# Kernel optimization log

Hardware: AMD Instinct MI355X
Metric: run time of the kernel (lower is better)

Reference implementation:

```python
import jax, jax.numpy as jnp
import numpy as np

EPS = 1e-5

def _ln(x, g, b):
    mu = jnp.mean(x, axis=-1, keepdims=True)
    var = jnp.mean((x - mu) ** 2, axis=-1, keepdims=True)
    return (x - mu) * jax.lax.rsqrt(var + EPS) * g + b

def setup_inputs() -> dict:
    key = jax.random.key(0)
    B, V, I, H = 32, 48, 24, 768
    ks = jax.random.split(key, 10)
    s = 0.02
    return {
        'variables': jax.random.normal(ks[0], (B, V, H), jnp.float32),
        'interventions': jax.random.normal(ks[1], (B, I, H), jnp.float32),
        # variable_encoder: Linear(H,H) + LayerNorm(H)
        'W_enc': jax.random.normal(ks[2], (H, H), jnp.float32) * s,
        'b_enc': jnp.zeros((H,), jnp.float32),
        'g_enc': jnp.ones((H,), jnp.float32),
        'be_enc': jnp.zeros((H,), jnp.float32),
        # graph_generator: Linear(2H,H) + LN(H) + ReLU + Linear(H,1) + Sigmoid
        'Wg1': jax.random.normal(ks[3], (2 * H, H), jnp.float32) * s,
        'bg1': jnp.zeros((H,), jnp.float32),
        'g_g': jnp.ones((H,), jnp.float32),
        'b_g': jnp.zeros((H,), jnp.float32),
        'Wg2': jax.random.normal(ks[4], (H, 1), jnp.float32) * s,
        'bg2': jnp.zeros((1,), jnp.float32),
        # intervention_predictor: Linear(2H,H) + LN(H) + ReLU + Linear(H,H)
        'Wi1': jax.random.normal(ks[5], (2 * H, H), jnp.float32) * s,
        'bi1': jnp.zeros((H,), jnp.float32),
        'g_i': jnp.ones((H,), jnp.float32),
        'b_i': jnp.zeros((H,), jnp.float32),
        'Wi2': jax.random.normal(ks[6], (H, H), jnp.float32) * s,
        'bi2': jnp.zeros((H,), jnp.float32),
    }

def reference(variables, interventions, W_enc, b_enc, g_enc, be_enc,
              Wg1, bg1, g_g, b_g, Wg2, bg2, Wi1, bi1, g_i, b_i, Wi2, bi2):
    H = variables.shape[-1]
    V = variables.shape[1]
    # variable encoder: Linear + LayerNorm + ReLU
    enc = jax.nn.relu(_ln(variables @ W_enc + b_enc, g_enc, be_enc))  # [B,V,H]

    # graph generator over all ordered pairs (i,j): concat([enc_i, enc_j]) @ Wg1
    # split Wg1 so the concat-matmul becomes two small GEMMs + broadcast add
    hi = jnp.einsum('bvh,hk->bvk', enc, Wg1[:H])   # contribution of enc_i
    hj = jnp.einsum('bvh,hk->bvk', enc, Wg1[H:])   # contribution of enc_j
    h = jax.nn.relu(_ln(hi[:, :, None, :] + hj[:, None, :, :] + bg1, g_g, b_g))  # [B,V,V,H]
    score = jax.nn.sigmoid(jnp.squeeze(h @ Wg2, -1) + bg2[0])  # [B,V,V]
    # diagonal (i==j) is never written in the original -> stays zero
    causal_graph = score * (1.0 - jnp.eye(V, dtype=score.dtype))

    # intervention predictor: concat([intervention_i, enc_j]) -> MLP
    ha = jnp.einsum('bih,hk->bik', interventions, Wi1[:H])  # [B,I,H]
    hb = jnp.einsum('bvh,hk->bvk', enc, Wi1[H:])            # [B,V,H]
    h2 = jax.nn.relu(_ln(ha[:, :, None, :] + hb[:, None, :, :] + bi1, g_i, b_i))  # [B,I,V,H]
    effects = h2 @ Wi2 + bi2  # [B,I,V,H]

    return (effects, causal_graph, enc)
```

## Files before the change

### kernel.cpp

```cpp
#include <hip/hip_runtime.h>
#include <math.h>

#define Bp 32
#define Vp 48
#define Ip 24
#define Hp 768
#define EPS 1e-5f

#define EFFECTS_SIZE (Bp*Ip*Vp*Hp)
#define GRAPH_SIZE   (Bp*Vp*Vp)
#define ENC_SIZE     (Bp*Vp*Hp)
#define MS           (Hp*Hp)

typedef __attribute__((ext_vector_type(8))) short short8;
typedef __attribute__((ext_vector_type(4))) float floatx4;
typedef __attribute__((ext_vector_type(2))) float floatx2;
typedef __attribute__((ext_vector_type(4))) unsigned int uintx4;

__device__ __forceinline__ unsigned short f2bf(float f) {
    unsigned int u = __float_as_uint(f);
    u += 0x7fffu + ((u >> 16) & 1u);
    return (unsigned short)(u >> 16);
}
__device__ __forceinline__ unsigned int f2bf2(float a, float b) {
    return (unsigned int)f2bf(a) | ((unsigned int)f2bf(b) << 16);
}

__device__ __forceinline__ uintx4 ln8(floatx4 xa, floatx4 xb, float mu, float rs,
                                      floatx4 ga, floatx4 gb, floatx4 ba, floatx4 bb)
{
    float y0 = fmaxf((xa.x - mu) * rs * ga.x + ba.x, 0.f);
    float y1 = fmaxf((xa.y - mu) * rs * ga.y + ba.y, 0.f);
    float y2 = fmaxf((xa.z - mu) * rs * ga.z + ba.z, 0.f);
    float y3 = fmaxf((xa.w - mu) * rs * ga.w + ba.w, 0.f);
    float y4 = fmaxf((xb.x - mu) * rs * gb.x + bb.x, 0.f);
    float y5 = fmaxf((xb.y - mu) * rs * gb.y + bb.y, 0.f);
    float y6 = fmaxf((xb.z - mu) * rs * gb.z + bb.z, 0.f);
    float y7 = fmaxf((xb.w - mu) * rs * gb.w + bb.w, 0.f);
    uintx4 v;
    v.x = f2bf2(y0, y1); v.y = f2bf2(y2, y3);
    v.z = f2bf2(y4, y5); v.w = f2bf2(y6, y7);
    return v;
}

__global__ __launch_bounds__(256) void pack_weights(
    const float* __restrict__ W_enc, const float* __restrict__ Wg1,
    const float* __restrict__ Wi1, const float* __restrict__ Wi2,
    unsigned short* __restrict__ packed)
{
    const int bid = blockIdx.x;
    const int m = bid / 288;
    const int rem = bid - m * 288;
    const int T = rem / 6;
    const int u = rem - T * 6;
    const float* src;
    switch (m) {
        case 0: src = W_enc; break;
        case 1: src = Wg1; break;
        case 2: src = Wg1 + Hp * Hp; break;
        case 3: src = Wi1 + Hp * Hp; break;
        case 4: src = Wi1; break;
        default: src = Wi2; break;
    }
    unsigned short* dst = packed + (size_t)m * MS;
    const int lane = threadIdx.x & 63;
    const int kq = threadIdx.x >> 6;
    const int col = T * 16 + (lane & 15);
    const int krow0 = (lane >> 4) * 8;
    const int kb = kq + 4 * u;
    unsigned int w[4];
#pragma unroll
    for (int p2 = 0; p2 < 4; ++p2) {
        float f0 = src[(size_t)(kb * 32 + krow0 + 2 * p2)     * Hp + col];
        float f1 = src[(size_t)(kb * 32 + krow0 + 2 * p2 + 1) * Hp + col];
        w[p2] = f2bf2(f0, f1);
    }
    uintx4 v; v.x = w[0]; v.y = w[1]; v.z = w[2]; v.w = w[3];
    *(uintx4*)(dst + ((size_t)(T * 24 + kb) * 64 + lane) * 8) = v;
}

__global__ __launch_bounds__(256) void convert_inputs(
    const float* __restrict__ vars, const float* __restrict__ intv,
    const float* __restrict__ bg1, const float* __restrict__ bi1,
    unsigned short* __restrict__ varb, unsigned short* __restrict__ intvb,
    float* __restrict__ bias2304)
{
    const int p = blockIdx.x * 256 + threadIdx.x;
    const int VPn = ENC_SIZE / 2;
    if (p < VPn) {
        float2 f = ((const float2*)vars)[p];
        ((unsigned int*)varb)[p] = f2bf2(f.x, f.y);
    } else {
        int q = p - VPn;
        float2 f = ((const float2*)intv)[q];
        ((unsigned int*)intvb)[q] = f2bf2(f.x, f.y);
    }
    if (blockIdx.x == 0) {
        for (int t = threadIdx.x; t < 2304; t += 256)
            bias2304[t] = (t < 768) ? 0.0f : (t < 1536 ? bg1[t - 768] : bi1[t - 1536]);
    }
}

__global__ __launch_bounds__(256) void gemm32(
    const unsigned short* __restrict__ A, const unsigned short* __restrict__ Bpk,
    const float* __restrict__ bias, float* __restrict__ C, int ldc)
{
    __shared__ unsigned short Asl[2 * 24 * 64 * 8];
    const int tid = threadIdx.x, wave = tid >> 6, lane = tid & 63;
    const int m0 = blockIdx.x * 32;

#pragma unroll
    for (int uu = 0; uu < 12; ++uu) {
        const int s = tid + 256 * uu;
        const int mt = s / 1536;
        const int r2 = s - mt * 1536;
        const int kb = r2 >> 6;
        const int L  = r2 & 63;
        uintx4 v = *(const uintx4*)(A + (size_t)(m0 + mt * 16 + (L & 15)) * Hp
                                      + kb * 32 + (L >> 4) * 8);
        *(uintx4*)(&Asl[((mt * 24 + kb) * 64 + (L ^ (kb & 7))) * 8]) = v;
    }
    __syncthreads();

    const int mrow = lane & 15, kq = lane >> 4;
    const int rot = ((blockIdx.x * 5 + blockIdx.y) & 7) * 3;
    const int wavep = (wave + blockIdx.x) & 3;
    const int Tg0 = blockIdx.y * 12 + wavep * 3;
    const unsigned short* Bbase = Bpk + (size_t)Tg0 * 12288 + lane * 8;

    const floatx4 z = {0.f, 0.f, 0.f, 0.f};
    floatx4 acc[2][3];
#pragma unroll
    for (int mt = 0; mt < 2; ++mt)
#pragma unroll
        for (int nt = 0; nt < 3; ++nt) acc[mt][nt] = z;

    short8 bbuf[4][3], abuf[2][2];
#pragma unroll
    for (int d = 0; d < 3; ++d) {
        int kc = d + rot; if (kc >= 24) kc -= 24;
#pragma unroll
        for (int nt = 0; nt < 3; ++nt)
            bbuf[d][nt] = *(const short8*)(Bbase + (size_t)nt * 12288 + kc * 512);
    }
    {
        int kc = rot;
#pragma unroll
        for (int mt = 0; mt < 2; ++mt)
            abuf[0][mt] = *(const short8*)(&Asl[((mt * 24 + kc) * 64 + (lane ^ (kc & 7))) * 8]);
    }

#pragma unroll
    for (int kb = 0; kb < 24; ++kb) {
        if (kb + 3 < 24) {
            int kc = kb + 3 + rot; if (kc >= 24) kc -= 24;
#pragma unroll
            for (int nt = 0; nt < 3; ++nt)
                bbuf[(kb + 3) & 3][nt] =
                    *(const short8*)(Bbase + (size_t)nt * 12288 + kc * 512);
        }
        if (kb + 1 < 24) {
            int kc = kb + 1 + rot; if (kc >= 24) kc -= 24;
#pragma unroll
            for (int mt = 0; mt < 2; ++mt)
                abuf[(kb + 1) & 1][mt] = *(const short8*)(
                    &Asl[((mt * 24 + kc) * 64 + (lane ^ (kc & 7))) * 8]);
        }
        __builtin_amdgcn_s_setprio(1);
#pragma unroll
        for (int mt = 0; mt < 2; ++mt)
#pragma unroll
            for (int nt = 0; nt < 3; ++nt)
                acc[mt][nt] = __builtin_amdgcn_mfma_f32_16x16x32_bf16(
                    abuf[kb & 1][mt], bbuf[kb & 3][nt], acc[mt][nt], 0, 0, 0);
        __builtin_amdgcn_s_setprio(0);
    }

#pragma unroll
    for (int nt = 0; nt < 3; ++nt) {
        const int colg = (Tg0 + nt) * 16 + mrow;
        const float bv = bias ? bias[colg] : 0.0f;
#pragma unroll
        for (int mt = 0; mt < 2; ++mt)
#pragma unroll
            for (int r = 0; r < 4; ++r)
                C[(size_t)(m0 + mt * 16 + kq * 4 + r) * ldc + colg] = acc[mt][nt][r] + bv;
    }
}

__global__ __launch_bounds__(256) void ln_relu(
    const float* __restrict__ pre, const float* __restrict__ g,
    const float* __restrict__ be, float* __restrict__ encf,
    unsigned short* __restrict__ encb)
{
    const int wave = threadIdx.x >> 6, lane = threadIdx.x & 63;
    const int row = blockIdx.x * 4 + wave;
    const float2* rp = (const float2*)(pre + (size_t)row * Hp);
    float2 x[6]; float s = 0.f, q = 0.f;
#pragma unroll
    for (int c = 0; c < 6; ++c) {
        x[c] = rp[lane + 64 * c];
        s += x[c].x + x[c].y;
        q += x[c].x * x[c].x + x[c].y * x[c].y;
    }
#pragma unroll
    for (int m = 1; m < 64; m <<= 1) { s += __shfl_xor(s, m, 64); q += __shfl_xor(q, m, 64); }
    const float mu = s * (1.0f / Hp);
    const float var = q * (1.0f / Hp) - mu * mu;
    const float rs = rsqrtf(var + EPS);
    floatx2* of = (floatx2*)(encf + (size_t)row * Hp);
    unsigned int* ob = (unsigned int*)(encb + (size_t)row * Hp);
#pragma unroll
    for (int c = 0; c < 6; ++c) {
        const float2 g2 = ((const float2*)g)[lane + 64 * c];
        const float2 b2 = ((const float2*)be)[lane + 64 * c];
        float y0 = fmaxf((x[c].x - mu) * rs * g2.x + b2.x, 0.f);
        float y1 = fmaxf((x[c].y - mu) * rs * g2.y + b2.y, 0.f);
        floatx2 y; y.x = y0; y.y = y1;
        __builtin_nontemporal_store(y, &of[lane + 64 * c]);
        ob[lane + 64 * c] = f2bf2(y0, y1);
    }
}

__global__ __launch_bounds__(256) void graph_kernel(
    const float* __restrict__ ws2, const float* __restrict__ gg_,
    const float* __restrict__ bb_, const float* __restrict__ Wg2,
    const float* __restrict__ bg2, float* __restrict__ out)
{
    const int wave = threadIdx.x >> 6, lane = threadIdx.x & 63;
    const int p = blockIdx.x;
    const int b = p / Vp, i = p - b * Vp;
    const floatx4* hi4 = (const floatx4*)(ws2 + (size_t)p * 2304);
    const floatx4* gg4 = (const floatx4*)gg_;
    const floatx4* bb4 = (const floatx4*)bb_;
    const floatx4* w24 = (const floatx4*)Wg2;
    floatx4 ri[3], gg[3], bb[3], w2[3];
#pragma unroll
    for (int c = 0; c < 3; ++c) {
        const int k = lane + 64 * c;
        ri[c] = hi4[k]; gg[c] = gg4[k]; bb[c] = bb4[k]; w2[c] = w24[k];
    }
    const float bg2v = bg2[0];
    const int j0 = wave * 12;
    for (int jj = 0; jj < 12; jj += 2) {
        const int jA = j0 + jj, jB = jA + 1;
        const floatx4* hjA = (const floatx4*)(ws2 + (size_t)(b * Vp + jA) * 2304 + 768);
        const floatx4* hjB = (const floatx4*)(ws2 + (size_t)(b * Vp + jB) * 2304 + 768);
        floatx4 xA[3], xB[3];
        float sA = 0.f, qA = 0.f, sB = 0.f, qB = 0.f;
#pragma unroll
        for (int c = 0; c < 3; ++c) {
            const int k = lane + 64 * c;
            xA[c] = ri[c] + hjA[k];
            xB[c] = ri[c] + hjB[k];
            sA += xA[c].x + xA[c].y + xA[c].z + xA[c].w;
            qA += xA[c].x * xA[c].x + xA[c].y * xA[c].y + xA[c].z * xA[c].z + xA[c].w * xA[c].w;
            sB += xB[c].x + xB[c].y + xB[c].z + xB[c].w;
            qB += xB[c].x * xB[c].x + xB[c].y * xB[c].y + xB[c].z * xB[c].z + xB[c].w * xB[c].w;
        }
#pragma unroll
        for (int m = 1; m < 64; m <<= 1) {
            sA += __shfl_xor(sA, m, 64); qA += __shfl_xor(qA, m, 64);
            sB += __shfl_xor(sB, m, 64); qB += __shfl_xor(qB, m, 64);
        }
        const float muA = sA * (1.0f / Hp);
        const float rsA = rsqrtf(qA * (1.0f / Hp) - muA * muA + EPS);
        const float muB = sB * (1.0f / Hp);
        const float rsB = rsqrtf(qB * (1.0f / Hp) - muB * muB + EPS);
        float pdA = 0.f, pdB = 0.f;
#pragma unroll
        for (int c = 0; c < 3; ++c) {
            float yA0 = fmaxf((xA[c].x - muA) * rsA * gg[c].x + bb[c].x, 0.f);
            float yA1 = fmaxf((xA[c].y - muA) * rsA * gg[c].y + bb[c].y, 0.f);
            float yA2 = fmaxf((xA[c].z - muA) * rsA * gg[c].z + bb[c].z, 0.f);
            float yA3 = fmaxf((xA[c].w - muA) * rsA * gg[c].w + bb[c].w, 0.f);
            pdA = fmaf(yA0, w2[c].x, pdA); pdA = fmaf(yA1, w2[c].y, pdA);
            pdA = fmaf(yA2, w2[c].z, pdA); pdA = fmaf(yA3, w2[c].w, pdA);
            float yB0 = fmaxf((xB[c].x - muB) * rsB * gg[c].x + bb[c].x, 0.f);
            float yB1 = fmaxf((xB[c].y - muB) * rsB * gg[c].y + bb[c].y, 0.f);
            float yB2 = fmaxf((xB[c].z - muB) * rsB * gg[c].z + bb[c].z, 0.f);
            float yB3 = fmaxf((xB[c].w - muB) * rsB * gg[c].w + bb[c].w, 0.f);
            pdB = fmaf(yB0, w2[c].x, pdB); pdB = fmaf(yB1, w2[c].y, pdB);
            pdB = fmaf(yB2, w2[c].z, pdB); pdB = fmaf(yB3, w2[c].w, pdB);
        }
#pragma unroll
        for (int m = 1; m < 64; m <<= 1) {
            pdA += __shfl_xor(pdA, m, 64);
            pdB += __shfl_xor(pdB, m, 64);
        }
        if (lane == 0) {
            float scA = (i == jA) ? 0.0f : 1.0f / (1.0f + expf(-(pdA + bg2v)));
            float scB = (i == jB) ? 0.0f : 1.0f / (1.0f + expf(-(pdB + bg2v)));
            out[(size_t)p * Vp + jA] = scA;
            out[(size_t)p * Vp + jB] = scB;
        }
    }
}

__global__ __launch_bounds__(512, 2) void effects96(
    const float* __restrict__ ha, const float* __restrict__ ws2,
    const float* __restrict__ g_i, const float* __restrict__ b_i,
    const unsigned short* __restrict__ Bpk, const float* __restrict__ bi2,
    float* __restrict__ out)
{
    __shared__ unsigned short Asl[6 * 24 * 64 * 8];
    const int tid = threadIdx.x, wave = tid >> 6, lane = tid & 63;
    const int bid = blockIdx.x;
    const int pair = bid >> 1, nhalf = bid & 1;
    const int b = pair / 12;
    const int bi0 = b * Ip + (pair - b * 12) * 2;
    const int half = lane >> 5, hl = lane & 31;

    {
        const floatx4* ha0 = (const floatx4*)(ha + (size_t)bi0 * Hp);
        const floatx4* ha1 = (const floatx4*)(ha + (size_t)(bi0 + 1) * Hp);
        const floatx4* gp = (const floatx4*)g_i;
        const floatx4* bp = (const floatx4*)b_i;
        floatx4 hv0[6], hv1[6], gv[6], bv[6];
#pragma unroll
        for (int t = 0; t < 3; ++t) {
            hv0[2*t] = ha0[2*hl + 64*t];  hv0[2*t+1] = ha0[2*hl + 1 + 64*t];
            hv1[2*t] = ha1[2*hl + 64*t];  hv1[2*t+1] = ha1[2*hl + 1 + 64*t];
            gv[2*t]  = gp[2*hl + 64*t];   gv[2*t+1]  = gp[2*hl + 1 + 64*t];
            bv[2*t]  = bp[2*hl + 64*t];   bv[2*t+1]  = bp[2*hl + 1 + 64*t];
        }

#pragma unroll
        for (int p = 0; p < 3; ++p) {
            const int j = wave * 6 + 2 * p + half;
            const floatx4* hbp = (const floatx4*)(ws2 + (size_t)(b * Vp + j) * 2304 + 1536);
            floatx4 x0[6], x1[6];
            float s0 = 0.f, q0 = 0.f, s1 = 0.f, q1 = 0.f;
#pragma unroll
            for (int t = 0; t < 3; ++t) {
                const floatx4 hA = hbp[2*hl + 64*t];
                const floatx4 hB = hbp[2*hl + 1 + 64*t];
                x0[2*t]   = hv0[2*t]   + hA;  x0[2*t+1] = hv0[2*t+1] + hB;
                x1[2*t]   = hv1[2*t]   + hA;  x1[2*t+1] = hv1[2*t+1] + hB;
            }
#pragma unroll
            for (int c = 0; c < 6; ++c) {
                s0 += x0[c].x + x0[c].y + x0[c].z + x0[c].w;
                q0 += x0[c].x*x0[c].x + x0[c].y*x0[c].y + x0[c].z*x0[c].z + x0[c].w*x0[c].w;
                s1 += x1[c].x + x1[c].y + x1[c].z + x1[c].w;
                q1 += x1[c].x*x1[c].x + x1[c].y*x1[c].y + x1[c].z*x1[c].z + x1[c].w*x1[c].w;
            }
#pragma unroll
            for (int m = 1; m < 32; m <<= 1) {
                s0 += __shfl_xor(s0, m, 64); q0 += __shfl_xor(q0, m, 64);
                s1 += __shfl_xor(s1, m, 64); q1 += __shfl_xor(q1, m, 64);
            }
            const float mu0 = s0 * (1.0f / Hp);
            const float rs0 = rsqrtf(q0 * (1.0f / Hp) - mu0 * mu0 + EPS);
            const float mu1 = s1 * (1.0f / Hp);
            const float rs1 = rsqrtf(q1 * (1.0f / Hp) - mu1 * mu1 + EPS);
            const int mt0 = j >> 4, mt1 = 3 + mt0, mr = j & 15;
#pragma unroll
            for (int t = 0; t < 3; ++t) {
                const int cpk = hl + 32 * t;
                const int kb = cpk >> 2, kq2 = cpk & 3;
                const int swz = (kq2 * 16 + mr) ^ (kb & 7);
                uintx4 v0 = ln8(x0[2*t], x0[2*t+1], mu0, rs0,
                                gv[2*t], gv[2*t+1], bv[2*t], bv[2*t+1]);
                *(uintx4*)(&Asl[((mt0 * 24 + kb) * 64 + swz) * 8]) = v0;
                uintx4 v1 = ln8(x1[2*t], x1[2*t+1], mu1, rs1,
                                gv[2*t], gv[2*t+1], bv[2*t], bv[2*t+1]);
                *(uintx4*)(&Asl[((mt1 * 24 + kb) * 64 + swz) * 8]) = v1;
            }
        }
    }
    __syncthreads();

    const int mrow = lane & 15, kq = lane >> 4;
    const int rot = (pair & 7) * 3;
    const int wavep = (wave + pair) & 7;
    const int Tg0 = nhalf * 24 + wavep * 3;
    const unsigned short* Bbase = Bpk + (size_t)Tg0 * 12288 + lane * 8;

    const floatx4 z = {0.f, 0.f, 0.f, 0.f};
    floatx4 acc[6][3];
#pragma unroll
    for (int mt = 0; mt < 6; ++mt)
#pragma unroll
        for (int nt = 0; nt < 3; ++nt) acc[mt][nt] = z;

    short8 bbuf[4][3], abuf[2][6];
#pragma unroll
    for (int d = 0; d < 3; ++d) {
        int kc = d + rot; if (kc >= 24) kc -= 24;
#pragma unroll
        for (int nt = 0; nt < 3; ++nt)
            bbuf[d][nt] = *(const short8*)(Bbase + (size_t)nt * 12288 + kc * 512);
    }
    {
        int kc = rot;
#pragma unroll
        for (int mt = 0; mt < 6; ++mt)
            abuf[0][mt] = *(const short8*)(&Asl[((mt * 24 + kc) * 64 + (lane ^ (kc & 7))) * 8]);
    }

#pragma unroll
    for (int kb = 0; kb < 24; ++kb) {
        if (kb + 3 < 24) {
            int kc = kb + 3 + rot; if (kc >= 24) kc -= 24;
#pragma unroll
            for (int nt = 0; nt < 3; ++nt)
                bbuf[(kb + 3) & 3][nt] =
                    *(const short8*)(Bbase + (size_t)nt * 12288 + kc * 512);
        }
        if (kb + 1 < 24) {
            int kc = kb + 1 + rot; if (kc >= 24) kc -= 24;
#pragma unroll
            for (int mt = 0; mt < 6; ++mt)
                abuf[(kb + 1) & 1][mt] = *(const short8*)(
                    &Asl[((mt * 24 + kc) * 64 + (lane ^ (kc & 7))) * 8]);
        }
        __builtin_amdgcn_s_setprio(1);
#pragma unroll
        for (int mt = 0; mt < 6; ++mt)
#pragma unroll
            for (int nt = 0; nt < 3; ++nt)
                acc[mt][nt] = __builtin_amdgcn_mfma_f32_16x16x32_bf16(
                    abuf[kb & 1][mt], bbuf[kb & 3][nt], acc[mt][nt], 0, 0, 0);
        __builtin_amdgcn_s_setprio(0);
    }

#pragma unroll
    for (int nt = 0; nt < 3; ++nt) {
        const int colg = (Tg0 + nt) * 16 + mrow;
        const float biasv = bi2[colg];
#pragma unroll
        for (int mt = 0; mt < 6; ++mt) {
#pragma unroll
            for (int r = 0; r < 4; ++r) {
                const int rr = mt * 16 + kq * 4 + r;
                __builtin_nontemporal_store(
                    acc[mt][nt][r] + biasv,
                    &out[(size_t)(bi0 * 48 + rr) * Hp + colg]);
            }
        }
    }
}

extern "C" void kernel_launch(void* const* d_in, const int* in_sizes, int n_in,
                              void* d_out, int out_size, void* d_ws, size_t ws_size,
                              hipStream_t stream) {
    const float* variables     = (const float*)d_in[0];
    const float* interventions = (const float*)d_in[1];
    const float* W_enc  = (const float*)d_in[2];
    const float* b_enc  = (const float*)d_in[3];
    const float* g_enc  = (const float*)d_in[4];
    const float* be_enc = (const float*)d_in[5];
    const float* Wg1 = (const float*)d_in[6];
    const float* bg1 = (const float*)d_in[7];
    const float* g_g = (const float*)d_in[8];
    const float* b_g = (const float*)d_in[9];
    const float* Wg2 = (const float*)d_in[10];
    const float* bg2 = (const float*)d_in[11];
    const float* Wi1 = (const float*)d_in[12];
    const float* bi1 = (const float*)d_in[13];
    const float* g_i = (const float*)d_in[14];
    const float* b_i = (const float*)d_in[15];
    const float* Wi2 = (const float*)d_in[16];
    const float* bi2 = (const float*)d_in[17];

    float* out = (float*)d_out;
    float* effects = out;
    float* graph = out + EFFECTS_SIZE;
    float* enc_f = out + EFFECTS_SIZE + GRAPH_SIZE;

    char* wsb = (char*)d_ws;
    unsigned short* packedW = (unsigned short*)wsb;
    float* ws2  = (float*)(wsb + 7077888);
    float* pre1 = ws2;
    float* ha   = (float*)(wsb + 7077888 + 14155776);
    unsigned short* varb  = (unsigned short*)(wsb + 23592960);
    unsigned short* intvb = (unsigned short*)(wsb + 25952256);
    unsigned short* encb  = (unsigned short*)(wsb + 27131904);
    float* bias2304 = (float*)(wsb + 29491200);

    pack_weights<<<1728, 256, 0, stream>>>(W_enc, Wg1, Wi1, Wi2, packedW);
    convert_inputs<<<3456, 256, 0, stream>>>(variables, interventions, bg1, bi1,
                                             varb, intvb, bias2304);
    gemm32<<<dim3(48, 4), 256, 0, stream>>>(varb, packedW, b_enc, pre1, Hp);
    ln_relu<<<384, 256, 0, stream>>>(pre1, g_enc, be_enc, enc_f, encb);
    gemm32<<<dim3(48, 12), 256, 0, stream>>>(encb, packedW + (size_t)1 * MS,
                                             bias2304, ws2, 2304);
    gemm32<<<dim3(24, 4), 256, 0, stream>>>(intvb, packedW + (size_t)4 * MS,
                                            nullptr, ha, Hp);
    graph_kernel<<<Bp * Vp, 256, 0, stream>>>(ws2, g_g, b_g, Wg2, bg2, graph);
    effects96<<<768, 512, 0, stream>>>(ha, ws2, g_i, b_i,
                                       packedW + (size_t)5 * MS, bi2, effects);
}
```

Before: 279.4 us.

## Merge encoder and intervention GEMMs into one launch; rewrite graph kernel with LDS tiling

The intervention GEMM, which does not depend on the encoder output, now runs in the same launch as the encoder GEMM through a combined grid, saving a kernel launch and letting the two fill the GPU together. The graph scorer is rebuilt so each block handles 6 i-rows of one batch and stages the hj rows in swizzled shared memory. Each lane then computes one (i,j) pair instead of one wave per pair with shuffle reductions. This trades the shuffle overhead for repeated LDS passes and fewer, larger blocks (256 blocks, 48 of 64 lanes active).

```diff
diff --git a/kernel.cpp b/kernel.cpp
--- a/kernel.cpp
+++ b/kernel.cpp
@@ -101,13 +101,14 @@
     }
 }
 
-__global__ __launch_bounds__(256) void gemm32(
+__device__ __forceinline__ void gemm32_body(
+    unsigned short* Asl,
     const unsigned short* __restrict__ A, const unsigned short* __restrict__ Bpk,
-    const float* __restrict__ bias, float* __restrict__ C, int ldc)
-{
-    __shared__ unsigned short Asl[2 * 24 * 64 * 8];
+    const float* __restrict__ bias, float* __restrict__ C, int ldc,
+    int bx, int by)
+{
     const int tid = threadIdx.x, wave = tid >> 6, lane = tid & 63;
-    const int m0 = blockIdx.x * 32;
+    const int m0 = bx * 32;
 
 #pragma unroll
     for (int uu = 0; uu < 12; ++uu) {
@@ -123,9 +124,9 @@
     __syncthreads();
 
     const int mrow = lane & 15, kq = lane >> 4;
-    const int rot = ((blockIdx.x * 5 + blockIdx.y) & 7) * 3;
-    const int wavep = (wave + blockIdx.x) & 3;
-    const int Tg0 = blockIdx.y * 12 + wavep * 3;
+    const int rot = ((bx * 5 + by) & 7) * 3;
+    const int wavep = (wave + bx) & 3;
+    const int Tg0 = by * 12 + wavep * 3;
     const unsigned short* Bbase = Bpk + (size_t)Tg0 * 12288 + lane * 8;
 
     const floatx4 z = {0.f, 0.f, 0.f, 0.f};
@@ -185,6 +186,29 @@
 #pragma unroll
             for (int r = 0; r < 4; ++r)
                 C[(size_t)(m0 + mt * 16 + kq * 4 + r) * ldc + colg] = acc[mt][nt][r] + bv;
+    }
+}
+
+__global__ __launch_bounds__(256) void gemm32(
+    const unsigned short* __restrict__ A, const unsigned short* __restrict__ Bpk,
+    const float* __restrict__ bias, float* __restrict__ C, int ldc)
+{
+    __shared__ unsigned short Asl[2 * 24 * 64 * 8];
+    gemm32_body(Asl, A, Bpk, bias, C, ldc, blockIdx.x, blockIdx.y);
+}
+
+__global__ __launch_bounds__(256) void gemm32_pair(
+    const unsigned short* __restrict__ A1, const unsigned short* __restrict__ B1,
+    const float* __restrict__ bias1, float* __restrict__ C1,
+    const unsigned short* __restrict__ A2, const unsigned short* __restrict__ B2,
+    float* __restrict__ C2)
+{
+    __shared__ unsigned short Asl[2 * 24 * 64 * 8];
+    if (blockIdx.y < 4) {
+        gemm32_body(Asl, A1, B1, bias1, C1, Hp, blockIdx.x, blockIdx.y);
+    } else {
+        if (blockIdx.x >= 24) return;
+        gemm32_body(Asl, A2, B2, nullptr, C2, Hp, blockIdx.x, blockIdx.y - 4);
     }
 }
 
@@ -222,78 +246,92 @@
     }
 }
 
-__global__ __launch_bounds__(256) void graph_kernel(
+__global__ __launch_bounds__(384) void graph_v2(
     const float* __restrict__ ws2, const float* __restrict__ gg_,
     const float* __restrict__ bb_, const float* __restrict__ Wg2,
     const float* __restrict__ bg2, float* __restrict__ out)
 {
-    const int wave = threadIdx.x >> 6, lane = threadIdx.x & 63;
-    const int p = blockIdx.x;
-    const int b = p / Vp, i = p - b * Vp;
-    const floatx4* hi4 = (const floatx4*)(ws2 + (size_t)p * 2304);
-    const floatx4* gg4 = (const floatx4*)gg_;
-    const floatx4* bb4 = (const floatx4*)bb_;
-    const floatx4* w24 = (const floatx4*)Wg2;
-    floatx4 ri[3], gg[3], bb[3], w2[3];
-#pragma unroll
-    for (int c = 0; c < 3; ++c) {
-        const int k = lane + 64 * c;
-        ri[c] = hi4[k]; gg[c] = gg4[k]; bb[c] = bb4[k]; w2[c] = w24[k];
-    }
-    const float bg2v = bg2[0];
-    const int j0 = wave * 12;
-    for (int jj = 0; jj < 12; jj += 2) {
-        const int jA = j0 + jj, jB = jA + 1;
-        const floatx4* hjA = (const floatx4*)(ws2 + (size_t)(b * Vp + jA) * 2304 + 768);
-        const floatx4* hjB = (const floatx4*)(ws2 + (size_t)(b * Vp + jB) * 2304 + 768);
-        floatx4 xA[3], xB[3];
-        float sA = 0.f, qA = 0.f, sB = 0.f, qB = 0.f;
-#pragma unroll
-        for (int c = 0; c < 3; ++c) {
-            const int k = lane + 64 * c;
-            xA[c] = ri[c] + hjA[k];
-            xB[c] = ri[c] + hjB[k];
-            sA += xA[c].x + xA[c].y + xA[c].z + xA[c].w;
-            qA += xA[c].x * xA[c].x + xA[c].y * xA[c].y + xA[c].z * xA[c].z + xA[c].w * xA[c].w;
-            sB += xB[c].x + xB[c].y + xB[c].z + xB[c].w;
-            qB += xB[c].x * xB[c].x + xB[c].y * xB[c].y + xB[c].z * xB[c].z + xB[c].w * xB[c].w;
-        }
-#pragma unroll
-        for (int m = 1; m < 64; m <<= 1) {
-            sA += __shfl_xor(sA, m, 64); qA += __shfl_xor(qA, m, 64);
-            sB += __shfl_xor(sB, m, 64); qB += __shfl_xor(qB, m, 64);
-        }
-        const float muA = sA * (1.0f / Hp);
-        const float rsA = rsqrtf(qA * (1.0f / Hp) - muA * muA + EPS);
-        const float muB = sB * (1.0f / Hp);
-        const float rsB = rsqrtf(qB * (1.0f / Hp) - muB * muB + EPS);
-        float pdA = 0.f, pdB = 0.f;
-#pragma unroll
-        for (int c = 0; c < 3; ++c) {
-            float yA0 = fmaxf((xA[c].x - muA) * rsA * gg[c].x + bb[c].x, 0.f);
-            float yA1 = fmaxf((xA[c].y - muA) * rsA * gg[c].y + bb[c].y, 0.f);
-            float yA2 = fmaxf((xA[c].z - muA) * rsA * gg[c].z + bb[c].z, 0.f);
-            float yA3 = fmaxf((xA[c].w - muA) * rsA * gg[c].w + bb[c].w, 0.f);
-            pdA = fmaf(yA0, w2[c].x, pdA); pdA = fmaf(yA1, w2[c].y, pdA);
-            pdA = fmaf(yA2, w2[c].z, pdA); pdA = fmaf(yA3, w2[c].w, pdA);
-            float yB0 = fmaxf((xB[c].x - muB) * rsB * gg[c].x + bb[c].x, 0.f);
-            float yB1 = fmaxf((xB[c].y - muB) * rsB * gg[c].y + bb[c].y, 0.f);
-            float yB2 = fmaxf((xB[c].z - muB) * rsB * gg[c].z + bb[c].z, 0.f);
-            float yB3 = fmaxf((xB[c].w - muB) * rsB * gg[c].w + bb[c].w, 0.f);
-            pdB = fmaf(yB0, w2[c].x, pdB); pdB = fmaf(yB1, w2[c].y, pdB);
-            pdB = fmaf(yB2, w2[c].z, pdB); pdB = fmaf(yB3, w2[c].w, pdB);
-        }
-#pragma unroll
-        for (int m = 1; m < 64; m <<= 1) {
-            pdA += __shfl_xor(pdA, m, 64);
-            pdB += __shfl_xor(pdB, m, 64);
-        }
-        if (lane == 0) {
-            float scA = (i == jA) ? 0.0f : 1.0f / (1.0f + expf(-(pdA + bg2v)));
-            float scB = (i == jB) ? 0.0f : 1.0f / (1.0f + expf(-(pdB + bg2v)));
-            out[(size_t)p * Vp + jA] = scA;
-            out[(size_t)p * Vp + jB] = scB;
-        }
+    __shared__ floatx4 HJ[96 * 64];
+    __shared__ floatx4 HI[6 * 192];
+    __shared__ floatx4 Gc[192];
+    __shared__ floatx4 Bc[192];
+    __shared__ floatx4 W2c[192];
+    const int tid = threadIdx.x, wave = tid >> 6, lane = tid & 63;
+    const int b = blockIdx.x >> 3, ig = blockIdx.x & 7;
+    const floatx4* w4 = (const floatx4*)ws2;
+
+    for (int idx = tid; idx < 6 * 192; idx += 384) {
+        const int i = idx / 192, c = idx - i * 192;
+        HI[idx] = w4[(size_t)(b * 48 + ig * 6 + i) * 576 + c];
+    }
+    for (int c = tid; c < 192; c += 384) {
+        Gc[c]  = ((const floatx4*)gg_)[c];
+        Bc[c]  = ((const floatx4*)bb_)[c];
+        W2c[c] = ((const floatx4*)Wg2)[c];
+    }
+    for (int idx = tid; idx < 48 * 96; idx += 384) {
+        const int j = idx / 96, c = idx - j * 96;
+        HJ[c * 64 + (j ^ (c & 7))] = w4[(size_t)(b * 48 + j) * 576 + 192 + c];
+    }
+    __syncthreads();
+
+    float s = 0.f, q = 0.f, pd = 0.f, mu = 0.f, rs = 0.f;
+
+    if (lane < 48) {
+#pragma unroll 4
+        for (int c = 0; c < 96; ++c) {
+            const floatx4 x = HI[wave * 192 + c] + HJ[c * 64 + (lane ^ (c & 7))];
+            s += x.x + x.y + x.z + x.w;
+            q += x.x * x.x + x.y * x.y + x.z * x.z + x.w * x.w;
+        }
+    }
+    __syncthreads();
+    for (int idx = tid; idx < 48 * 96; idx += 384) {
+        const int j = idx / 96, c = idx - j * 96;
+        HJ[c * 64 + (j ^ (c & 7))] = w4[(size_t)(b * 48 + j) * 576 + 192 + 96 + c];
+    }
+    __syncthreads();
+
+    if (lane < 48) {
+#pragma unroll 4
+        for (int c = 0; c < 96; ++c) {
+            const floatx4 x = HI[wave * 192 + 96 + c] + HJ[c * 64 + (lane ^ (c & 7))];
+            s += x.x + x.y + x.z + x.w;
+            q += x.x * x.x + x.y * x.y + x.z * x.z + x.w * x.w;
+        }
+        mu = s * (1.0f / Hp);
+        rs = rsqrtf(q * (1.0f / Hp) - mu * mu + EPS);
+#pragma unroll 2
+        for (int c = 0; c < 96; ++c) {
+            const floatx4 x = HI[wave * 192 + 96 + c] + HJ[c * 64 + (lane ^ (c & 7))];
+            const floatx4 g = Gc[96 + c], b2 = Bc[96 + c], w = W2c[96 + c];
+            pd += fmaxf((x.x - mu) * rs * g.x + b2.x, 0.f) * w.x;
+            pd += fmaxf((x.y - mu) * rs * g.y + b2.y, 0.f) * w.y;
+            pd += fmaxf((x.z - mu) * rs * g.z + b2.z, 0.f) * w.z;
+            pd += fmaxf((x.w - mu) * rs * g.w + b2.w, 0.f) * w.w;
+        }
+    }
+    __syncthreads();
+    for (int idx = tid; idx < 48 * 96; idx += 384) {
+        const int j = idx / 96, c = idx - j * 96;
+        HJ[c * 64 + (j ^ (c & 7))] = w4[(size_t)(b * 48 + j) * 576 + 192 + c];
+    }
+    __syncthreads();
+
+    if (lane < 48) {
+#pragma unroll 2
+        for (int c = 0; c < 96; ++c) {
+            const floatx4 x = HI[wave * 192 + c] + HJ[c * 64 + (lane ^ (c & 7))];
+            const floatx4 g = Gc[c], b2 = Bc[c], w = W2c[c];
+            pd += fmaxf((x.x - mu) * rs * g.x + b2.x, 0.f) * w.x;
+            pd += fmaxf((x.y - mu) * rs * g.y + b2.y, 0.f) * w.y;
+            pd += fmaxf((x.z - mu) * rs * g.z + b2.z, 0.f) * w.z;
+            pd += fmaxf((x.w - mu) * rs * g.w + b2.w, 0.f) * w.w;
+        }
+        const int ii = ig * 6 + wave;
+        const float v = pd + bg2[0];
+        const float sc = (ii == lane) ? 0.f : 1.f / (1.f + expf(-v));
+        out[((size_t)b * 48 + ii) * 48 + lane] = sc;
     }
 }
 
@@ -482,13 +520,12 @@
     pack_weights<<<1728, 256, 0, stream>>>(W_enc, Wg1, Wi1, Wi2, packedW);
     convert_inputs<<<3456, 256, 0, stream>>>(variables, interventions, bg1, bi1,
                                              varb, intvb, bias2304);
-    gemm32<<<dim3(48, 4), 256, 0, stream>>>(varb, packedW, b_enc, pre1, Hp);
+    gemm32_pair<<<dim3(48, 8), 256, 0, stream>>>(varb, packedW, b_enc, pre1,
+                                                 intvb, packedW + (size_t)4 * MS, ha);
     ln_relu<<<384, 256, 0, stream>>>(pre1, g_enc, be_enc, enc_f, encb);
     gemm32<<<dim3(48, 12), 256, 0, stream>>>(encb, packedW + (size_t)1 * MS,
                                              bias2304, ws2, 2304);
-    gemm32<<<dim3(24, 4), 256, 0, stream>>>(intvb, packedW + (size_t)4 * MS,
-                                            nullptr, ha, Hp);
-    graph_kernel<<<Bp * Vp, 256, 0, stream>>>(ws2, g_g, b_g, Wg2, bg2, graph);
+    graph_v2<<<256, 384, 0, stream>>>(ws2, g_g, b_g, Wg2, bg2, graph);
     effects96<<<768, 512, 0, stream>>>(ha, ws2, g_i, b_i,
                                        packedW + (size_t)5 * MS, bi2, effects);
 }
```

Measured after the change: 298.5 us. +6.8%, slower.
